# Kernel tuning notes

Hardware: AMD Instinct MI355X
Metric: run time of the kernel (lower is better)

Reference implementation:

```python
import jax, jax.numpy as jnp
import numpy as np

B = 4194304  # batch rows
L = 4        # hidden width of LinearNNComplex


def _net(x3, W1, b1, W2, b2):
    # Linear(3->L) -> ReLU -> Linear(L->1) -> Sigmoid
    h = jax.nn.relu(x3 @ W1 + b1)          # [B, L]
    return jax.nn.sigmoid(h @ W2 + b2)     # [B, 1]


def setup_inputs() -> dict:
    key = jax.random.key(0)
    ks = jax.random.split(key, 14)
    x = jax.random.normal(ks[0], (B, 4), dtype=jnp.float32)
    # column 1 is the per-row dispatch selector in {0,1,2} (also used as a feature)
    sel = jax.random.randint(ks[1], (B,), 0, 3).astype(jnp.float32)
    x = x.at[:, 1].set(sel)
    def lin(k, fan_in, fan_out):
        return jax.random.normal(k, (fan_in, fan_out), dtype=jnp.float32) * 0.1
    inp = {"x": x}
    names = ["s", "u", "d"]  # straight / up / down nets
    for i, n in enumerate(names):
        inp[f"W{n}1"] = lin(ks[2 + 4 * i], 3, L)
        inp[f"b{n}1"] = jax.random.normal(ks[3 + 4 * i], (L,), dtype=jnp.float32) * 0.1
        inp[f"W{n}2"] = lin(ks[4 + 4 * i], L, 1)
        inp[f"b{n}2"] = jax.random.normal(ks[5 + 4 * i], (1,), dtype=jnp.float32) * 0.1
    return inp


def reference(x, Ws1, bs1, Ws2, bs2, Wu1, bu1, Wu2, bu2, Wd1, bd1, Wd2, bd2):
    x3 = x[:, :3]                 # input[:, :-1]
    sel = x[:, 1:2]               # dispatch column
    out_s = _net(x3, Ws1, bs1, Ws2, bs2)
    out_u = _net(x3, Wu1, bu1, Wu2, bu2)
    out_d = _net(x3, Wd1, bd1, Wd2, bd2)
    zero = jnp.zeros_like(out_s)  # rows matching no selector stay 0 (torch init)
    res = jnp.where(sel == 0.0, out_s,
          jnp.where(sel == 1.0, out_u,
          jnp.where(sel == 2.0, out_d, zero)))
    return res                    # [B, 1]
```

## Files before the change

### kernel.cpp

```cpp
#include <hip/hip_runtime.h>


#define ROWS 4

typedef float fvec4 __attribute__((ext_vector_type(4)));

__global__ __launch_bounds__(256) void Program_72902774882571_kernel(
    const float* __restrict__ x,
    const float* __restrict__ Ws1, const float* __restrict__ bs1,
    const float* __restrict__ Ws2, const float* __restrict__ bs2,
    const float* __restrict__ Wu1, const float* __restrict__ bu1,
    const float* __restrict__ Wu2, const float* __restrict__ bu2,
    const float* __restrict__ Wd1, const float* __restrict__ bd1,
    const float* __restrict__ Wd2, const float* __restrict__ bd2,
    float* __restrict__ out, int n)
{
    const int base = blockIdx.x * (256 * ROWS) + threadIdx.x;

    fvec4 xv[ROWS];
#pragma unroll
    for (int k = 0; k < ROWS; ++k) {
        const int i = base + k * 256;
        xv[k] = (fvec4){0.f, -1.f, 0.f, 0.f};
        if (i < n)
            xv[k] = __builtin_nontemporal_load(reinterpret_cast<const fvec4*>(x) + i);
    }

#pragma unroll
    for (int k = 0; k < ROWS; ++k) {
        const int i = base + k * 256;
        if (i >= n) continue;
        const float x0 = xv[k][0], x1 = xv[k][1], x2 = xv[k][2];

        const bool is_s = (x1 == 0.0f);
        const bool is_u = (x1 == 1.0f);
        const bool is_d = (x1 == 2.0f);

        auto pick = [&](float s, float u, float d) -> float {
            return is_s ? s : (is_u ? u : d);
        };

        float acc = pick(bs2[0], bu2[0], bd2[0]);
#pragma unroll
        for (int j = 0; j < 4; ++j) {
            float h = pick(bs1[j], bu1[j], bd1[j]);
            h = fmaf(x0, pick(Ws1[0 * 4 + j], Wu1[0 * 4 + j], Wd1[0 * 4 + j]), h);
            h = fmaf(x1, pick(Ws1[1 * 4 + j], Wu1[1 * 4 + j], Wd1[1 * 4 + j]), h);
            h = fmaf(x2, pick(Ws1[2 * 4 + j], Wu1[2 * 4 + j], Wd1[2 * 4 + j]), h);
            h = fmaxf(h, 0.0f);
            acc = fmaf(h, pick(Ws2[j], Wu2[j], Wd2[j]), acc);
        }
        const float e = __builtin_amdgcn_exp2f(acc * -1.44269504088896340736f);
        const float o = __builtin_amdgcn_rcpf(1.0f + e);

        const float r = (is_s | is_u | is_d) ? o : 0.0f;

        __builtin_nontemporal_store(r, &out[i]);
    }
}

extern "C" void kernel_launch(void* const* d_in, const int* in_sizes, int n_in,
                              void* d_out, int out_size, void* d_ws, size_t ws_size,
                              hipStream_t stream) {
    const float* x   = (const float*)d_in[0];
    const float* Ws1 = (const float*)d_in[1];
    const float* bs1 = (const float*)d_in[2];
    const float* Ws2 = (const float*)d_in[3];
    const float* bs2 = (const float*)d_in[4];
    const float* Wu1 = (const float*)d_in[5];
    const float* bu1 = (const float*)d_in[6];
    const float* Wu2 = (const float*)d_in[7];
    const float* bu2 = (const float*)d_in[8];
    const float* Wd1 = (const float*)d_in[9];
    const float* bd1 = (const float*)d_in[10];
    const float* Wd2 = (const float*)d_in[11];
    const float* bd2 = (const float*)d_in[12];

    const int n = out_size;
    const int block = 256;
    const int rows_per_block = block * ROWS;
    const int grid = (n + rows_per_block - 1) / rows_per_block;

    Program_72902774882571_kernel<<<grid, block, 0, stream>>>(
        x, Ws1, bs1, Ws2, bs2, Wu1, bu1, Wu2, bu2, Wd1, bd1, Wd2, bd2,
        (float*)d_out, n);
}
```

Measured before the change: 131.9 us.

## Compute all three nets with folded selector bias, drop bounds checks

Replaces per-weight three-way selects with computing all three small MLPs branch-free. The selector column's contribution is folded into the first-layer bias, since x1 is constant per branch. ROWS goes from 4 to 8, and a template variant drops bounds checks when n divides evenly. Input loads switch from nontemporal to ordinary loads. The kernel is memory-bound at about 80 MB of traffic, so the extra ALU work probably matters little, and the folding is exact only for rows that match a selector.

```diff
diff --git a/kernel.cpp b/kernel.cpp
--- a/kernel.cpp
+++ b/kernel.cpp
@@ -1,10 +1,11 @@
 #include <hip/hip_runtime.h>
 
 
-#define ROWS 4
+#define ROWS 8
 
 typedef float fvec4 __attribute__((ext_vector_type(4)));
 
+template <bool EXACT>
 __global__ __launch_bounds__(256) void Program_72902774882571_kernel(
     const float* __restrict__ x,
     const float* __restrict__ Ws1, const float* __restrict__ bs1,
@@ -21,39 +22,43 @@
 #pragma unroll
     for (int k = 0; k < ROWS; ++k) {
         const int i = base + k * 256;
-        xv[k] = (fvec4){0.f, -1.f, 0.f, 0.f};
-        if (i < n)
-            xv[k] = __builtin_nontemporal_load(reinterpret_cast<const fvec4*>(x) + i);
+        if (EXACT || i < n)
+            xv[k] = reinterpret_cast<const fvec4*>(x)[i];
+        else
+            xv[k] = (fvec4){0.f, -1.f, 0.f, 0.f};
+    }
+
+    float bup[4], bdp[4];
+#pragma unroll
+    for (int j = 0; j < 4; ++j) {
+        bup[j] = bu1[j] + Wu1[4 + j];
+        bdp[j] = fmaf(2.0f, Wd1[4 + j], bd1[j]);
     }
 
 #pragma unroll
     for (int k = 0; k < ROWS; ++k) {
         const int i = base + k * 256;
-        if (i >= n) continue;
+        if (!EXACT && i >= n) continue;
         const float x0 = xv[k][0], x1 = xv[k][1], x2 = xv[k][2];
 
-        const bool is_s = (x1 == 0.0f);
-        const bool is_u = (x1 == 1.0f);
-        const bool is_d = (x1 == 2.0f);
-
-        auto pick = [&](float s, float u, float d) -> float {
-            return is_s ? s : (is_u ? u : d);
-        };
-
-        float acc = pick(bs2[0], bu2[0], bd2[0]);
+        float as = bs2[0], au = bu2[0], ad = bd2[0];
 #pragma unroll
         for (int j = 0; j < 4; ++j) {
-            float h = pick(bs1[j], bu1[j], bd1[j]);
-            h = fmaf(x0, pick(Ws1[0 * 4 + j], Wu1[0 * 4 + j], Wd1[0 * 4 + j]), h);
-            h = fmaf(x1, pick(Ws1[1 * 4 + j], Wu1[1 * 4 + j], Wd1[1 * 4 + j]), h);
-            h = fmaf(x2, pick(Ws1[2 * 4 + j], Wu1[2 * 4 + j], Wd1[2 * 4 + j]), h);
-            h = fmaxf(h, 0.0f);
-            acc = fmaf(h, pick(Ws2[j], Wu2[j], Wd2[j]), acc);
+            const float hs = fmaf(x0, Ws1[j], fmaf(x2, Ws1[8 + j], bs1[j]));
+            const float hu = fmaf(x0, Wu1[j], fmaf(x2, Wu1[8 + j], bup[j]));
+            const float hd = fmaf(x0, Wd1[j], fmaf(x2, Wd1[8 + j], bdp[j]));
+            as = fmaf(fmaxf(hs, 0.f), Ws2[j], as);
+            au = fmaf(fmaxf(hu, 0.f), Wu2[j], au);
+            ad = fmaf(fmaxf(hd, 0.f), Wd2[j], ad);
         }
-        const float e = __builtin_amdgcn_exp2f(acc * -1.44269504088896340736f);
-        const float o = __builtin_amdgcn_rcpf(1.0f + e);
 
-        const float r = (is_s | is_u | is_d) ? o : 0.0f;
+        float a = (x1 == 2.0f) ? ad : 0.0f;
+        a = (x1 == 1.0f) ? au : a;
+        a = (x1 == 0.0f) ? as : a;
+        const float e = __builtin_amdgcn_exp2f(a * -1.44269504088896340736f);
+        float r = __builtin_amdgcn_rcpf(1.0f + e);
+        const bool valid = (x1 == 0.0f) | (x1 == 1.0f) | (x1 == 2.0f);
+        r = valid ? r : 0.0f;
 
         __builtin_nontemporal_store(r, &out[i]);
     }
@@ -81,7 +86,13 @@
     const int rows_per_block = block * ROWS;
     const int grid = (n + rows_per_block - 1) / rows_per_block;
 
-    Program_72902774882571_kernel<<<grid, block, 0, stream>>>(
-        x, Ws1, bs1, Ws2, bs2, Wu1, bu1, Wu2, bu2, Wd1, bd1, Wd2, bd2,
-        (float*)d_out, n);
+    if (n % rows_per_block == 0) {
+        Program_72902774882571_kernel<true><<<grid, block, 0, stream>>>(
+            x, Ws1, bs1, Ws2, bs2, Wu1, bu1, Wu2, bu2, Wd1, bd1, Wd2, bd2,
+            (float*)d_out, n);
+    } else {
+        Program_72902774882571_kernel<false><<<grid, block, 0, stream>>>(
+            x, Ws1, bs1, Ws2, bs2, Wu1, bu1, Wu2, bu2, Wd1, bd1, Wd2, bd2,
+            (float*)d_out, n);
+    }
 }
```

New measurement: 124.5 us. -5.7%, faster.
